# Optimization experiments

Measured on AMD Instinct MI355X. Metric: run time of the kernel, lower is better.

The kernel has to match this reference:

```python
import jax, jax.numpy as jnp
import numpy as np
from jax import lax
from jax.scipy.special import logsumexp

B, T, K, D = 16, 128, 1024, 768
APPROX_R = 0.1
LAMBD = 0.1
KP = int(APPROX_R * K)  # num_state_approx = 102


def setup_inputs() -> dict:
    key = jax.random.key(0)
    k0, k1, k2, k3 = jax.random.split(key, 4)
    x_emb = jax.random.normal(k0, (B, T, D), jnp.float32)
    # nn.Parameter(torch.normal(0, norm_scale_transition, [K, D]))
    state_matrix = 0.01 * jax.random.normal(k1, (K, D), jnp.float32)
    y = jax.random.randint(k2, (B, T), 0, K)
    y_lens = jax.random.randint(k3, (B,), 1, T + 1)
    return {"x_emb": x_emb, "state_matrix": state_matrix, "y": y, "y_lens": y_lens}


def _forward_sum(transition, emission, y_lens):
    # exact linear-chain CRF forward (logsumexp) scan. emission: [B,T,K]
    bsz = emission.shape[0]
    def step(alpha, em_t):
        new = logsumexp(alpha[:, :, None] + transition[None], axis=1) + em_t
        return new, new
    a0 = emission[:, 0]
    _, rest = lax.scan(step, a0, jnp.swapaxes(emission, 0, 1)[1:])
    alphas = jnp.concatenate([a0[None], rest], axis=0)  # [T,B,K]
    a_last = alphas[y_lens - 1, jnp.arange(bsz)]        # [B,K]
    return logsumexp(a_last, axis=-1)


def _approx_forward(state_matrix, emission, y_lens, kp):
    # restricted forward over the top-kp states (by emission potential) per
    # position; transitions among selected states computed on the fly from
    # state embeddings (avoids the full KxK transition).
    bsz = emission.shape[0]
    d = state_matrix.shape[1]
    em_top, idx = lax.top_k(emission, kp)   # [B,T,KP]
    st_sel = state_matrix[idx]              # [B,T,KP,D]
    def step(carry, inp):
        alpha, st_prev = carry
        em_t, st_t = inp
        trans_t = jnp.einsum('bid,bjd->bij', st_prev, st_t) / np.sqrt(d)
        new = logsumexp(alpha[:, :, None] + trans_t, axis=1) + em_t
        return (new, st_t), new
    a0 = em_top[:, 0]
    xs = (jnp.swapaxes(em_top, 0, 1)[1:], jnp.swapaxes(st_sel, 0, 1)[1:])
    _, rest = lax.scan(step, (a0, st_sel[:, 0]), xs)
    alphas = jnp.concatenate([a0[None], rest], axis=0)
    a_last = alphas[y_lens - 1, jnp.arange(bsz)]
    return logsumexp(a_last, axis=-1)


def _viterbi(transition, emission, y_lens):
    bsz, tlen, k = emission.shape
    def step(alpha, em_t):
        scores = alpha[:, :, None] + transition[None]
        bp = jnp.argmax(scores, axis=1).astype(jnp.int32)
        new = jnp.max(scores, axis=1) + em_t
        return new, (new, bp)
    a0 = emission[:, 0]
    _, (rest, bps) = lax.scan(step, a0, jnp.swapaxes(emission, 0, 1)[1:])
    alphas = jnp.concatenate([a0[None], rest], axis=0)  # [T,B,K]
    a_last = alphas[y_lens - 1, jnp.arange(bsz)]
    last_state = jnp.argmax(a_last, axis=-1).astype(jnp.int32)
    # bps[t] maps best state at t+1 -> state at t; pad to length T
    bps_pad = jnp.concatenate([bps, jnp.zeros((1, bsz, k), jnp.int32)], axis=0)
    def back(s, inp):
        t, bp_t = inp
        cand = jnp.take_along_axis(bp_t, s[:, None], axis=1)[:, 0]
        s_new = jnp.where(t == y_lens - 1, last_state,
                          jnp.where(t < y_lens - 1, cand, 0))
        return s_new, s_new
    ts = jnp.arange(tlen)[::-1]
    _, s_seq = lax.scan(back, jnp.zeros((bsz,), jnp.int32), (ts, bps_pad[::-1]))
    return jnp.swapaxes(s_seq[::-1], 0, 1)  # [B,T]


def _evaluate(y_pred, y, y_lens, mask_f):
    support = ((y > 0).astype(jnp.float32) * mask_f).sum()
    pred = ((y_pred > 0).astype(jnp.float32) * mask_f).sum()
    overlap = (((y_pred > 0) & (y > 0)).astype(jnp.float32) * mask_f).sum()
    acc = ((y_pred == y).astype(jnp.float32) * mask_f).sum() / y_lens.sum()
    prec = jnp.where(pred > 0, overlap / jnp.maximum(pred, 1.0), 0.0)
    recl = overlap / jnp.maximum(support, 1.0)
    f1 = jnp.where(prec > 0, 2 * prec * recl / jnp.maximum(prec + recl, 1e-12), 0.0)
    return acc, prec, recl, f1


def reference(x_emb, state_matrix, y, y_lens):
    d = x_emb.shape[-1]
    bsz, tlen = y.shape
    emission = jnp.einsum('btd,kd->btk', x_emb, state_matrix) / np.sqrt(d)
    transition = jnp.matmul(state_matrix, state_matrix.T) / np.sqrt(d)

    log_Z = _forward_sum(transition, emission, y_lens)
    log_Z_approx = _approx_forward(state_matrix, emission, y_lens, KP)

    # gold sequence log potential, masked by lengths
    pos = jnp.arange(tlen)
    mask = (pos[None, :] < y_lens[:, None])
    mask_f = mask.astype(jnp.float32)
    mask_tr = (pos[None, :tlen - 1] < (y_lens - 1)[:, None]).astype(jnp.float32)
    em_y = jnp.take_along_axis(emission, y[..., None], axis=-1)[..., 0]
    trans_y = transition[y[:, :-1], y[:, 1:]]
    log_y_potential = (em_y * mask_f).sum(-1) + (trans_y * mask_tr).sum(-1)

    seq_log_prob_exact = -(log_y_potential - log_Z).mean()
    seq_log_prob_approx = -(log_y_potential - log_Z_approx).mean()

    total_len = y_lens.sum()
    logp = jax.nn.log_softmax(emission, axis=-1)
    lp_y = jnp.take_along_axis(logp, y[..., None], axis=-1)[..., 0]
    seq_log_prob_local = (lp_y * mask_f).sum() / total_len
    max_prob = (jnp.max(jax.nn.softmax(emission, -1), -1) * mask_f).sum() / total_len

    # loss_type == 'approx_crf'
    loss = seq_log_prob_approx + LAMBD * seq_log_prob_local

    crf_output = _viterbi(transition, emission, y_lens)
    crf_acc, crf_prec, crf_recl, crf_f1 = _evaluate(crf_output, y, y_lens, mask_f)
    softmax_output = emission.argmax(-1)
    sm_acc, sm_prec, sm_recl, sm_f1 = _evaluate(softmax_output, y, y_lens, mask_f)

    return (loss, crf_output, log_Z.mean(), log_Z_approx.mean(),
            seq_log_prob_exact, seq_log_prob_local, max_prob,
            crf_acc, crf_f1, sm_acc, sm_f1)


if __name__ == '__main__':
    out = reference(**setup_inputs())
    print(out[0], out[2], out[3])
```

## Files before the change

kernel.cpp:

```cpp
#include <hip/hip_runtime.h>
#include <cstdint>
#include <cstddef>

typedef unsigned long long ull;
typedef unsigned int uint32;
typedef unsigned short u16;
typedef __attribute__((ext_vector_type(8))) short s8v;
typedef __attribute__((ext_vector_type(4))) float f32x4;


#define OFF_EM    ((size_t)0)
#define OFF_TR    ((size_t)2097152)
#define OFF_EXPTB ((size_t)3145728)
#define OFF_UPP   ((size_t)3670016)
#define OFF_APP   ((size_t)3735552)
#define OFF_ULST  ((size_t)3801088)
#define OFF_ALST  ((size_t)3817472)
#define OFF_UALST ((size_t)3833856)
#define OFF_ETOP  ((size_t)3835904)
#define OFF_ITOP  ((size_t)4044800)
#define OFF_RMAX  ((size_t)4253696)
#define OFF_RLSE  ((size_t)4255744)
#define OFF_SMP   ((size_t)4257792)
#define OFF_BP    ((size_t)4259840)
#define OFF_DONE  ((size_t)6356992)
#define OFF_EXPTT ((size_t)6367744)

__device__ __forceinline__ u16 f2bf(float f) {
  uint32 u = __builtin_bit_cast(uint32, f);
  u = (u + 0x7fffu + ((u >> 16) & 1u)) >> 16;
  return (u16)u;
}
__device__ __forceinline__ float bflo(uint32 w) {
  return __builtin_bit_cast(float, w << 16);
}
__device__ __forceinline__ void bfsplit(float v, u16& h, u16& l) {
  h = f2bf(v);
  float rh = __builtin_bit_cast(float, ((uint32)h) << 16);
  l = f2bf(v - rh);
}

__device__ __forceinline__ uint32 load_bypass_u32(const uint32* p) {
  return __hip_atomic_load(p, __ATOMIC_RELAXED, __HIP_MEMORY_SCOPE_AGENT);
}
__device__ __forceinline__ void store_bypass_u32(uint32* p, uint32 v) {
  __hip_atomic_store(p, v, __ATOMIC_RELAXED, __HIP_MEMORY_SCOPE_AGENT);
}
__device__ __forceinline__ void store_bypass_u16(u16* p, u16 v) {
  __hip_atomic_store(p, v, __ATOMIC_RELAXED, __HIP_MEMORY_SCOPE_AGENT);
}
__device__ __forceinline__ float load_bypass_f(const float* p) {
  return __hip_atomic_load(p, __ATOMIC_RELAXED, __HIP_MEMORY_SCOPE_AGENT);
}
__device__ __forceinline__ void store_bypass_f(float* p, float v) {
  __hip_atomic_store(p, v, __ATOMIC_RELAXED, __HIP_MEMORY_SCOPE_AGENT);
}
__device__ __forceinline__ void store_bypass_i(int* p, int v) {
  __hip_atomic_store(p, v, __ATOMIC_RELAXED, __HIP_MEMORY_SCOPE_AGENT);
}
__device__ __forceinline__ int load_bypass_i(const int* p) {
  return __hip_atomic_load(p, __ATOMIC_RELAXED, __HIP_MEMORY_SCOPE_AGENT);
}
__device__ __forceinline__ void cnt_add(uint32* p) {
  __hip_atomic_fetch_add(p, 1u, __ATOMIC_RELAXED, __HIP_MEMORY_SCOPE_AGENT);
}
__device__ __forceinline__ float4 ld_b128_sc1(const float4* p) {
  float4 r;
  asm volatile("global_load_dwordx4 %0, %1, off sc1" : "=v"(r) : "v"(p));
  return r;
}

__global__ __launch_bounds__(256) void gemm_kernel(
    const float* __restrict__ x, const float* __restrict__ stm,
    float* __restrict__ emission, float* __restrict__ transition,
    u16* __restrict__ expTb) {
  __shared__ float As[16][68];
  __shared__ float Bs[16][68];
  const int tid = threadIdx.x;
  const int tx = tid & 15, ty = tid >> 4;
  const int m0 = blockIdx.x * 64, n0 = blockIdx.y * 64;
  const int lr = tid >> 2;
  const int lc = (tid & 3) << 2;
  float acc[4][4] = {};
  const float* aptr;
  {
    int gr = m0 + lr;
    aptr = (gr < 2048) ? (x + (size_t)gr * 768) : (stm + (size_t)(gr - 2048) * 768);
  }
  const float* bptr = stm + (size_t)(n0 + lr) * 768;
  for (int k0 = 0; k0 < 768; k0 += 16) {
    float4 a4 = *(const float4*)(aptr + k0 + lc);
    float4 b4 = *(const float4*)(bptr + k0 + lc);
    __syncthreads();
    As[lc + 0][lr] = a4.x; As[lc + 1][lr] = a4.y; As[lc + 2][lr] = a4.z; As[lc + 3][lr] = a4.w;
    Bs[lc + 0][lr] = b4.x; Bs[lc + 1][lr] = b4.y; Bs[lc + 2][lr] = b4.z; Bs[lc + 3][lr] = b4.w;
    __syncthreads();
#pragma unroll
    for (int kk = 0; kk < 16; ++kk) {
      float a[4], b[4];
#pragma unroll
      for (int q = 0; q < 4; ++q) a[q] = As[kk][ty * 4 + q];
#pragma unroll
      for (int q = 0; q < 4; ++q) b[q] = Bs[kk][tx * 4 + q];
#pragma unroll
      for (int i2 = 0; i2 < 4; ++i2)
#pragma unroll
        for (int j2 = 0; j2 < 4; ++j2) acc[i2][j2] += a[i2] * b[j2];
    }
  }
  const float rs = 0.03608439182435161f;
#pragma unroll
  for (int i2 = 0; i2 < 4; ++i2) {
    int r = m0 + ty * 4 + i2;
#pragma unroll
    for (int j2 = 0; j2 < 4; ++j2) {
      int c = n0 + tx * 4 + j2;
      float v = acc[i2][j2] * rs;
      if (r < 2048) {
        emission[(size_t)r * 1024 + c] = v;
      } else {
        size_t o = (size_t)(r - 2048) * 1024 + c;
        transition[o] = v;
        expTb[o] = f2bf(expf(v));
      }
    }
  }
}

__global__ __launch_bounds__(256) void transT_kernel(
    const u16* __restrict__ src, u16* __restrict__ dst) {
  __shared__ u16 tile[64][65];
  const int bx = blockIdx.x * 64, by = blockIdx.y * 64;
  const int tx = threadIdx.x & 63, ty4 = threadIdx.x >> 6;
  for (int rr = ty4; rr < 64; rr += 4)
    tile[rr][tx] = src[(size_t)(bx + rr) * 1024 + by + tx];
  __syncthreads();
  for (int rr = ty4; rr < 64; rr += 4)
    dst[(size_t)(by + rr) * 1024 + bx + tx] = tile[tx][rr];
}

__global__ __launch_bounds__(256) void topk_kernel(
    const float* __restrict__ emission, float* __restrict__ em_top,
    int* __restrict__ top_idx, float* __restrict__ row_max,
    float* __restrict__ row_lse, int* __restrict__ sm_pred) {
  __shared__ float v[1024];
  __shared__ int ix[1024];
  __shared__ float rb[256];
  const int row = blockIdx.x;
  const int tid = threadIdx.x;
  const float* e = emission + (size_t)row * 1024;
  for (int p = tid; p < 1024; p += 256) { v[p] = e[p]; ix[p] = p; }
  __syncthreads();
  for (int k = 2; k <= 1024; k <<= 1) {
    for (int j = k >> 1; j > 0; j >>= 1) {
      for (int p = tid; p < 1024; p += 256) {
        int l = p ^ j;
        if (l > p) {
          float va = v[p], vb = v[l];
          int ia = ix[p], ib = ix[l];
          bool aBefore = (va > vb) || (va == vb && ia < ib);
          bool up = ((p & k) == 0);
          if (up ? !aBefore : aBefore) { v[p] = vb; v[l] = va; ix[p] = ib; ix[l] = ia; }
        }
      }
      __syncthreads();
    }
  }
  float mx = v[0];
  float s = 0.f;
  for (int p = tid; p < 1024; p += 256) s += expf(v[p] - mx);
  rb[tid] = s; __syncthreads();
  for (int w = 128; w > 0; w >>= 1) { if (tid < w) rb[tid] += rb[tid + w]; __syncthreads(); }
  if (tid == 0) {
    row_max[row] = mx;
    row_lse[row] = mx + logf(rb[0]);
    sm_pred[row] = ix[0];
  }
  for (int p = tid; p < 102; p += 256) {
    em_top[(size_t)row * 102 + p] = v[p];
    top_idx[(size_t)row * 102 + p] = ix[p];
  }
}

__global__ __launch_bounds__(256) void zero_kernel(uint32* __restrict__ done) {
  const int idx = blockIdx.x * 256 + threadIdx.x;
  store_bypass_u32(done + idx, 0u);
}

__global__ __launch_bounds__(512) void scan_kernel(
    const float* __restrict__ em, const float* __restrict__ tr,
    const u16* __restrict__ expTb, const u16* __restrict__ expTbT,
    const float* __restrict__ em_top, const int* __restrict__ top_idx,
    const int* __restrict__ y_lens,
    float* __restrict__ u_ring, float* __restrict__ av_ring,
    float* __restrict__ u_last, float* __restrict__ av_last,
    float* __restrict__ ua_last, int* __restrict__ bp,
    uint32* __restrict__ done, float* __restrict__ out_crf) {
  __shared__ ull SH[9232];
  const int bid = blockIdx.x, tid = threadIdx.x;
  uint32* cntF = done;
  uint32* cntV = done + 64;
  uint32* vdone = done + 640;

  if (bid < 8) {
    const int p = bid;
    int* stbF = (int*)(SH + 8192);
    if (tid < 16) stbF[tid] = y_lens[tid] - 1;
    const int l = tid & 63;
    const int lm = l & 15, lq = l >> 4;
    const int w2 = (tid >> 6) & 3;
    if (tid < 256) {
      const int m = tid >> 4;
      const int nn = p * 128 + ((tid & 15) << 3);
      const float* e0 = em + ((size_t)m << 17) + nn;
      u16* rh = (u16*)u_ring;
      const bool last0 = (y_lens[m] == 1);
#pragma unroll
      for (int q = 0; q < 8; ++q) {
        float v = expf(e0[q]);
        u16 h, lo2; bfsplit(v, h, lo2);
        store_bypass_u16(rh + m * 1024 + nn + q, h);
        store_bypass_u16(rh + 16384 + m * 1024 + nn + q, lo2);
        if (last0) u_last[(size_t)m * 1024 + nn + q] = v;
      }
      asm volatile("s_waitcnt vmcnt(0)" ::: "memory");
    }
    __syncthreads();
    if (tid == 0) cnt_add(cntF + 0);
    const char* Ab = (const char*)SH;
    const int offh = (lm << 11) + (lq << 4);
    const int axor = (lm & 7) << 4;
    const int nbase = p * 128 + w2 * 32;
    const u16* bq0 = expTbT + ((size_t)(nbase + lm) << 10) + (lq << 3);
    const u16* bq1 = bq0 + (16 << 10);
    for (int t = 1; t < 128; ++t) {
      if (tid == 0) {
        const uint32 tgt = (uint32)((((t - 1) >> 2) + 1) * 8);
        const uint32* cp = cntF + (((t - 1) & 3) << 4);
        while (load_bypass_u32(cp) < tgt) __builtin_amdgcn_s_sleep(1);
      }
      __syncthreads();
      {
        const float4* src = (const float4*)(u_ring + (size_t)((t - 1) & 3) * 16384);
        float4 dbuf[8];
#pragma unroll
        for (int q = 0; q < 8; ++q) dbuf[q] = ld_b128_sc1(src + (q << 9) + tid);
        asm volatile("s_waitcnt vmcnt(0)" ::: "memory");
        __builtin_amdgcn_sched_barrier(0);
#pragma unroll
        for (int q = 0; q < 8; ++q) {
          const int ob = ((q << 9) + tid) << 4;
          *(float4*)((char*)SH + (ob ^ (((ob >> 11) & 7) << 4))) = dbuf[q];
        }
      }
      __syncthreads();
      if (tid < 256) {
        f32x4 acc0a = {0.f, 0.f, 0.f, 0.f}, acc0b = {0.f, 0.f, 0.f, 0.f};
        f32x4 acc1a = {0.f, 0.f, 0.f, 0.f}, acc1b = {0.f, 0.f, 0.f, 0.f};
        for (int k0 = 0; k0 < 1024; k0 += 64) {
          const int o0 = (offh + (k0 << 1)) ^ axor;
          const int o1 = (offh + ((k0 + 32) << 1)) ^ axor;
          s8v ah0 = *(const s8v*)(Ab + o0);
          s8v al0 = *(const s8v*)(Ab + 32768 + o0);
          s8v ah1 = *(const s8v*)(Ab + o1);
          s8v al1 = *(const s8v*)(Ab + 32768 + o1);
          s8v b00 = *(const s8v*)(bq0 + k0);
          s8v b10 = *(const s8v*)(bq1 + k0);
          s8v b01 = *(const s8v*)(bq0 + k0 + 32);
          s8v b11 = *(const s8v*)(bq1 + k0 + 32);
          acc0a = __builtin_amdgcn_mfma_f32_16x16x32_bf16(ah0, b00, acc0a, 0, 0, 0);
          acc1a = __builtin_amdgcn_mfma_f32_16x16x32_bf16(ah0, b10, acc1a, 0, 0, 0);
          acc0b = __builtin_amdgcn_mfma_f32_16x16x32_bf16(ah1, b01, acc0b, 0, 0, 0);
          acc1b = __builtin_amdgcn_mfma_f32_16x16x32_bf16(ah1, b11, acc1b, 0, 0, 0);
          acc0a = __builtin_amdgcn_mfma_f32_16x16x32_bf16(al0, b00, acc0a, 0, 0, 0);
          acc1a = __builtin_amdgcn_mfma_f32_16x16x32_bf16(al0, b10, acc1a, 0, 0, 0);
          acc0b = __builtin_amdgcn_mfma_f32_16x16x32_bf16(al1, b01, acc0b, 0, 0, 0);
          acc1b = __builtin_amdgcn_mfma_f32_16x16x32_bf16(al1, b11, acc1b, 0, 0, 0);
        }
        u16* rh = (u16*)(u_ring + (size_t)(t & 3) * 16384);
        const float sc = 1.0f / 1024.0f;
#pragma unroll
        for (int r = 0; r < 4; ++r) {
          const int m = (lq << 2) + r;
          const size_t erow = (((size_t)m << 7) + t) << 10;
          {
            const int n = nbase + lm;
            float v = (acc0a[r] + acc0b[r]) * sc * expf(em[erow + n]);
            u16 h, lo2; bfsplit(v, h, lo2);
            store_bypass_u16(rh + m * 1024 + n, h);
            store_bypass_u16(rh + 16384 + m * 1024 + n, lo2);
            if (t == stbF[m]) u_last[(size_t)m * 1024 + n] = v;
          }
          {
            const int n = nbase + 16 + lm;
            float v = (acc1a[r] + acc1b[r]) * sc * expf(em[erow + n]);
            u16 h, lo2; bfsplit(v, h, lo2);
            store_bypass_u16(rh + m * 1024 + n, h);
            store_bypass_u16(rh + 16384 + m * 1024 + n, lo2);
            if (t == stbF[m]) u_last[(size_t)m * 1024 + n] = v;
          }
        }
        asm volatile("s_waitcnt vmcnt(0)" ::: "memory");
      }
      __syncthreads();
      if (tid == 0) cnt_add(cntF + ((t & 3) << 4));
    }
  } else if (bid < 136) {
    const int v = bid - 8;
    const int n0v = ((v & 7) << 7) + ((v >> 3) << 3);
    const int jj = tid & 7, g = tid >> 3;
    const int col = n0v + jj;
    ull* ppb = (ull*)((char*)SH + 65536);
    int* stb2 = (int*)((char*)SH + 73728);
    if (tid < 16) stb2[tid] = y_lens[tid] - 1;
    if (tid < 128) {
      const int jb = tid & 7, b = tid >> 3;
      const float e0 = em[((size_t)b << 17) + n0v + jb];
      store_bypass_f(av_ring + (size_t)(n0v + jb) * 16 + b, e0);
      if (y_lens[b] == 1) store_bypass_f(av_last + ((size_t)b << 10) + n0v + jb, e0);
      asm volatile("s_waitcnt vmcnt(0)" ::: "memory");
    }
    __syncthreads();
    if (tid == 0) cnt_add(cntV + ((v & 7) << 4));
    const char* stc = (const char*)SH;
    for (int t = 1; t < 128; ++t) {
      if (tid < 8) {
        const uint32 tgt = (uint32)((((t - 1) >> 2) + 1) * 16);
        const uint32* cp = cntV + (((((t - 1) & 3) << 3) + tid) << 4);
        while (load_bypass_u32(cp) < tgt) __builtin_amdgcn_s_sleep(1);
      }
      __syncthreads();
      {
        const float4* src = (const float4*)(av_ring + (size_t)((t - 1) & 3) * 16384);
        float4 dbuf[8];
#pragma unroll
        for (int q = 0; q < 8; ++q) dbuf[q] = ld_b128_sc1(src + (q << 9) + tid);
        asm volatile("s_waitcnt vmcnt(0)" ::: "memory");
        __builtin_amdgcn_sched_barrier(0);
#pragma unroll
        for (int q = 0; q < 8; ++q) {
          const int ob = ((q << 9) + tid) << 4;
          *(float4*)((char*)SH + (ob ^ (((ob >> 10) & 7) << 4))) = dbuf[q];
        }
      }
      __syncthreads();
      float mv[16]; int mi[16];
#pragma unroll
      for (int b = 0; b < 16; ++b) { mv[b] = -3.0e38f; mi[b] = 0x7fffffff; }
      const float* trc = tr + col;
      const int i0 = g << 4;
#pragma unroll 4
      for (int ii = 0; ii < 16; ++ii) {
        const int i = i0 + ii;
        const float tv = trc[(size_t)i << 10];
        const int ph = (i << 6) ^ (((i >> 4) & 7) << 4);
        const f32x4 s0 = *(const f32x4*)(stc + (ph ^ 0));
        const f32x4 s1 = *(const f32x4*)(stc + (ph ^ 16));
        const f32x4 s2 = *(const f32x4*)(stc + (ph ^ 32));
        const f32x4 s3 = *(const f32x4*)(stc + (ph ^ 48));
#pragma unroll
        for (int b = 0; b < 4; ++b) {
          float c0 = s0[b] + tv; if (c0 > mv[b])      { mv[b] = c0;      mi[b] = i; }
          float c1 = s1[b] + tv; if (c1 > mv[b + 4])  { mv[b + 4] = c1;  mi[b + 4] = i; }
          float c2 = s2[b] + tv; if (c2 > mv[b + 8])  { mv[b + 8] = c2;  mi[b + 8] = i; }
          float c3 = s3[b] + tv; if (c3 > mv[b + 12]) { mv[b + 12] = c3; mi[b + 12] = i; }
        }
      }
#pragma unroll
      for (int d = 8; d <= 32; d <<= 1) {
#pragma unroll
        for (int b = 0; b < 16; ++b) {
          float ov = __shfl_xor(mv[b], d);
          int oi = __shfl_xor(mi[b], d);
          if (ov > mv[b] || (ov == mv[b] && oi < mi[b])) { mv[b] = ov; mi[b] = oi; }
        }
      }
      if ((tid & 63) < 8) {
        const int wv = tid >> 6;
#pragma unroll
        for (int b = 0; b < 16; ++b) {
          ull pk = ((ull)(uint32)mi[b] << 32) | (ull)__builtin_bit_cast(uint32, mv[b]);
          ppb[(b << 6) + (wv << 3) + jj] = pk;
        }
      }
      __syncthreads();
      if (tid < 128) {
        const int jb = tid & 7, b = tid >> 3;
        const int cf = n0v + jb;
        float bmv = -3.0e38f; int bmi = 0x7fffffff;
#pragma unroll
        for (int w = 0; w < 8; ++w) {
          ull pk = ppb[(b << 6) + (w << 3) + jb];
          float pv = __builtin_bit_cast(float, (uint32)pk);
          int pi = (int)(pk >> 32);
          if (pv > bmv || (pv == bmv && pi < bmi)) { bmv = pv; bmi = pi; }
        }
        const float nv = bmv + em[((((size_t)b << 7) + t) << 10) + cf];
        store_bypass_f(av_ring + (size_t)(t & 3) * 16384 + (size_t)cf * 16 + b, nv);
        store_bypass_i(bp + ((size_t)t << 14) + ((size_t)b << 10) + cf, bmi);
        if (t == stb2[b]) store_bypass_f(av_last + ((size_t)b << 10) + cf, nv);
        asm volatile("s_waitcnt vmcnt(0)" ::: "memory");
      }
      __syncthreads();
      if (tid == 0) cnt_add(cntV + ((((t & 3) << 3) + (v & 7)) << 4));
    }
    if (tid == 0) cnt_add(vdone);
    if (v == 0) {
      if (tid == 0) {
        while (load_bypass_u32(vdone) < 128u) __builtin_amdgcn_s_sleep(1);
      }
      __syncthreads();
      const int wv = tid >> 6, lh = tid & 63;
      const int hb = lh >> 5, hl = lh & 31;
      const int b = wv * 2 + hb;
      const int tbb = y_lens[b] - 1;
      for (int t2 = tbb + 1 + hl; t2 < 128; t2 += 32) out_crf[(b << 7) + t2] = 0.f;
      float bv = -3.0e38f; int bi = 0x7fffffff;
      for (int q = 0; q < 32; ++q) {
        const int i = (q << 5) + hl;
        const float val = load_bypass_f(av_last + ((size_t)b << 10) + i);
        if (val > bv || (val == bv && i < bi)) { bv = val; bi = i; }
      }
#pragma unroll
      for (int d = 1; d < 32; d <<= 1) {
        float ov = __shfl_xor(bv, d, 32);
        int oi = __shfl_xor(bi, d, 32);
        if (ov > bv || (ov == bv && oi < bi)) { bv = ov; bi = oi; }
      }
      if (hl == 0) {
        int sx = bi;
        out_crf[(b << 7) + tbb] = (float)sx;
        for (int t2 = tbb - 1; t2 >= 0; --t2) {
          sx = load_bypass_i(bp + ((size_t)(t2 + 1) << 14) + ((size_t)b << 10) + sx);
          out_crf[(b << 7) + t2] = (float)sx;
        }
      }
    }
  } else {
    const int b = bid - 136;
    const int tb = y_lens[b] - 1;
    const int j2 = tid & 127, h2 = tid >> 7;
    float* sua0 = (float*)SH;
    float* sua1 = sua0 + 104;
    int* sidxp = (int*)(sua0 + 208);
    int* sidxc = sidxp + 104;
    float* aps = (float*)(sidxc + 104);
    if (tid < 102) {
      float vv = expf(em_top[(size_t)(b * 128) * 102 + tid]);
      sua0[tid] = vv;
      if (tb == 0) ua_last[b * 102 + tid] = vv;
    }
    __syncthreads();
    for (int t = 1; t < 128; ++t) {
      if (tid < 102) sidxp[tid] = top_idx[((size_t)b * 128 + (t - 1)) * 102 + tid];
      else if (tid >= 256 && tid < 358)
        sidxc[tid - 256] = top_idx[((size_t)b * 128 + t) * 102 + (tid - 256)];
      __syncthreads();
      float acc2 = 0.f;
      float* up = (t & 1) ? sua0 : sua1;
      float* cur = (t & 1) ? sua1 : sua0;
      if (j2 < 102) {
        const int colc = sidxc[j2];
        const int ia = h2 * 26;
        const int ib2 = (ia + 26 < 102) ? ia + 26 : 102;
        for (int i = ia; i < ib2; ++i)
          acc2 += up[i] * bflo((uint32)expTb[(size_t)sidxp[i] * 1024 + colc]);
      }
      if (h2 > 0 && j2 < 102) aps[(h2 - 1) * 104 + j2] = acc2;
      __syncthreads();
      if (h2 == 0 && j2 < 102) {
        acc2 += aps[j2] + aps[104 + j2] + aps[208 + j2];
        const float e = em_top[((size_t)b * 128 + t) * 102 + j2];
        const float nv = acc2 * expf(e) * (1.0f / 102.0f);
        cur[j2] = nv;
        if (t == tb) ua_last[b * 102 + j2] = nv;
      }
      __syncthreads();
    }
  }
}

__device__ __forceinline__ float blk_sum(float v, float* rb, int tid) {
  rb[tid] = v; __syncthreads();
  for (int w = 128; w > 0; w >>= 1) { if (tid < w) rb[tid] += rb[tid + w]; __syncthreads(); }
  float r = rb[0]; __syncthreads();
  return r;
}

__global__ __launch_bounds__(256) void finalize_kernel(
    const float* __restrict__ emission, const float* __restrict__ transition,
    const float* __restrict__ u_last, const float* __restrict__ ua_last,
    const float* __restrict__ row_max, const float* __restrict__ row_lse,
    const int* __restrict__ sm_pred, const int* __restrict__ y,
    const int* __restrict__ y_lens, float* __restrict__ d_out) {
  __shared__ float rb[256];
  __shared__ float sZ[16], sZa[16], sLogy[16];
  const int tid = threadIdx.x;
  const float* out_crf = d_out + 1;
  for (int b = 0; b < 16; ++b) {
    const int tb = y_lens[b] - 1;
    float p = 0.f;
    for (int i = tid; i < 1024; i += 256) p += u_last[(size_t)b * 1024 + i];
    p = blk_sum(p, rb, tid);
    if (tid == 0) sZ[b] = logf(p) + (float)tb * 6.931471805599453f;
    float q = 0.f;
    for (int i = tid; i < 102; i += 256) q += ua_last[(size_t)b * 102 + i];
    q = blk_sum(q, rb, tid);
    if (tid == 0) sZa[b] = logf(q) + (float)tb * 4.624972813284271f;
  }
  if (tid < 16) sLogy[tid] = 0.f;
  __syncthreads();
  float a_local = 0, a_maxp = 0, c_sup = 0, c_pred = 0, c_ov = 0, c_match = 0;
  float s_predc = 0, s_ov = 0, s_match = 0;
  for (int r = tid; r < 2048; r += 256) {
    const int b = r >> 7, t = r & 127;
    const int L = y_lens[b];
    if (t < L) {
      const int yv = y[r];
      const float em_y = emission[(size_t)r * 1024 + yv];
      const float lse = row_lse[r];
      a_local += em_y - lse;
      a_maxp += expf(row_max[r] - lse);
      float term = em_y;
      if (t < L - 1) term += transition[(size_t)yv * 1024 + y[r + 1]];
      atomicAdd(&sLogy[b], term);
      const float ypos = (yv > 0) ? 1.f : 0.f;
      c_sup += ypos;
      const int cs = (int)out_crf[r];
      c_pred += (cs > 0) ? 1.f : 0.f;
      c_ov += ((cs > 0) && (yv > 0)) ? 1.f : 0.f;
      c_match += (cs == yv) ? 1.f : 0.f;
      const int ss = sm_pred[r];
      s_predc += (ss > 0) ? 1.f : 0.f;
      s_ov += ((ss > 0) && (yv > 0)) ? 1.f : 0.f;
      s_match += (ss == yv) ? 1.f : 0.f;
    }
  }
  __syncthreads();
  a_local = blk_sum(a_local, rb, tid);
  a_maxp = blk_sum(a_maxp, rb, tid);
  c_sup = blk_sum(c_sup, rb, tid);
  c_pred = blk_sum(c_pred, rb, tid);
  c_ov = blk_sum(c_ov, rb, tid);
  c_match = blk_sum(c_match, rb, tid);
  s_predc = blk_sum(s_predc, rb, tid);
  s_ov = blk_sum(s_ov, rb, tid);
  s_match = blk_sum(s_match, rb, tid);
  if (tid == 0) {
    float tl = 0.f;
    for (int b = 0; b < 16; ++b) tl += (float)y_lens[b];
    float mZ = 0, mZa = 0, dE = 0, dA = 0;
    for (int b = 0; b < 16; ++b) {
      mZ += sZ[b]; mZa += sZa[b];
      dE += sLogy[b] - sZ[b];
      dA += sLogy[b] - sZa[b];
    }
    mZ *= (1.f / 16.f); mZa *= (1.f / 16.f);
    const float sle = -dE * (1.f / 16.f);
    const float sla = -dA * (1.f / 16.f);
    const float slocal = a_local / tl;
    const float maxp = a_maxp / tl;
    const float loss = sla + 0.1f * slocal;
    const float crf_acc = c_match / tl;
    const float crf_prec = (c_pred > 0.f) ? (c_ov / fmaxf(c_pred, 1.f)) : 0.f;
    const float crf_recl = c_ov / fmaxf(c_sup, 1.f);
    const float crf_f1 = (crf_prec > 0.f)
        ? (2.f * crf_prec * crf_recl / fmaxf(crf_prec + crf_recl, 1e-12f)) : 0.f;
    const float sm_acc = s_match / tl;
    const float sm_prec = (s_predc > 0.f) ? (s_ov / fmaxf(s_predc, 1.f)) : 0.f;
    const float sm_recl = s_ov / fmaxf(c_sup, 1.f);
    const float sm_f1 = (sm_prec > 0.f)
        ? (2.f * sm_prec * sm_recl / fmaxf(sm_prec + sm_recl, 1e-12f)) : 0.f;
    d_out[0] = loss;
    d_out[2049] = mZ;
    d_out[2050] = mZa;
    d_out[2051] = sle;
    d_out[2052] = slocal;
    d_out[2053] = maxp;
    d_out[2054] = crf_acc;
    d_out[2055] = crf_f1;
    d_out[2056] = sm_acc;
    d_out[2057] = sm_f1;
  }
}

extern "C" void kernel_launch(void* const* d_in, const int* in_sizes, int n_in,
                              void* d_out, int out_size, void* d_ws, size_t ws_size,
                              hipStream_t stream) {
  const float* x = (const float*)d_in[0];
  const float* stm = (const float*)d_in[1];
  const int* y = (const int*)d_in[2];
  const int* yl = (const int*)d_in[3];
  float* out = (float*)d_out;
  float* ws = (float*)d_ws;

  float* emission = ws + OFF_EM;
  float* transition = ws + OFF_TR;
  u16* expTb = (u16*)(ws + OFF_EXPTB);
  u16* expTbT = (u16*)(ws + OFF_EXPTT);
  float* u_ring = ws + OFF_UPP;
  float* av_ring = ws + OFF_APP;
  float* u_last = ws + OFF_ULST;
  float* av_last = ws + OFF_ALST;
  float* ua_last = ws + OFF_UALST;
  float* em_top = ws + OFF_ETOP;
  int* top_idx = (int*)(ws + OFF_ITOP);
  float* row_max = ws + OFF_RMAX;
  float* row_lse = ws + OFF_RLSE;
  int* sm_pred = (int*)(ws + OFF_SMP);
  int* bp = (int*)(ws + OFF_BP);
  uint32* done = (uint32*)(ws + OFF_DONE);

  zero_kernel<<<4, 256, 0, stream>>>(done);
  gemm_kernel<<<dim3(48, 16), 256, 0, stream>>>(x, stm, emission, transition, expTb);
  transT_kernel<<<dim3(16, 16), 256, 0, stream>>>(expTb, expTbT);
  topk_kernel<<<2048, 256, 0, stream>>>(emission, em_top, top_idx, row_max, row_lse, sm_pred);
  scan_kernel<<<152, 512, 0, stream>>>(emission, transition, expTb, expTbT, em_top, top_idx,
                                       yl, u_ring, av_ring, u_last, av_last, ua_last,
                                       bp, done, out + 1);
  finalize_kernel<<<1, 256, 0, stream>>>(emission, transition, u_last, ua_last,
                                         row_max, row_lse, sm_pred, y, yl, out);
}
```

Before: 1.887 ms.

## Replace counter-based inter-block sync with poisoned ring-buffer data flags

Drops the per-step atomic counters and spin-waits in the persistent scan kernel. Consumers now reload ring-buffer entries until none holds a poison sentinel, and each block re-poisons the slot two steps ahead. The forward ring also packs the bf16 hi/lo halves into one 32-bit word, halving the number of stores, and the consumer unpacks them into LDS. This removes the store drain, barrier and atomic round-trip on every step, but relies on relaxed store visibility ordering and on the sentinel never colliding with real data.

```diff
diff --git a/kernel.cpp b/kernel.cpp
--- a/kernel.cpp
+++ b/kernel.cpp
@@ -8,6 +8,9 @@
 typedef __attribute__((ext_vector_type(8))) short s8v;
 typedef __attribute__((ext_vector_type(4))) float f32x4;
 
+
+#define POISON32 0xFFFFFFFFu
+#define POISON64 0xFFFFFFFFFFFFFFFFull
 
 #define OFF_EM    ((size_t)0)
 #define OFF_TR    ((size_t)2097152)
@@ -46,7 +49,7 @@
 __device__ __forceinline__ void store_bypass_u32(uint32* p, uint32 v) {
   __hip_atomic_store(p, v, __ATOMIC_RELAXED, __HIP_MEMORY_SCOPE_AGENT);
 }
-__device__ __forceinline__ void store_bypass_u16(u16* p, u16 v) {
+__device__ __forceinline__ void store_bypass_u64(ull* p, ull v) {
   __hip_atomic_store(p, v, __ATOMIC_RELAXED, __HIP_MEMORY_SCOPE_AGENT);
 }
 __device__ __forceinline__ float load_bypass_f(const float* p) {
@@ -182,9 +185,12 @@
   }
 }
 
-__global__ __launch_bounds__(256) void zero_kernel(uint32* __restrict__ done) {
+__global__ __launch_bounds__(256) void poison_kernel(
+    ull* __restrict__ uring, ull* __restrict__ aring, uint32* __restrict__ done) {
   const int idx = blockIdx.x * 256 + threadIdx.x;
-  store_bypass_u32(done + idx, 0u);
+  store_bypass_u64(uring + idx, POISON64);
+  store_bypass_u64(aring + idx, POISON64);
+  if (idx == 0) store_bypass_u32(done, 0u);
 }
 
 __global__ __launch_bounds__(512) void scan_kernel(
@@ -198,9 +204,7 @@
     uint32* __restrict__ done, float* __restrict__ out_crf) {
   __shared__ ull SH[9232];
   const int bid = blockIdx.x, tid = threadIdx.x;
-  uint32* cntF = done;
-  uint32* cntV = done + 64;
-  uint32* vdone = done + 640;
+  uint32* vdone = done;
 
   if (bid < 8) {
     const int p = bid;
@@ -213,20 +217,17 @@
       const int m = tid >> 4;
       const int nn = p * 128 + ((tid & 15) << 3);
       const float* e0 = em + ((size_t)m << 17) + nn;
-      u16* rh = (u16*)u_ring;
+      uint32* rw = (uint32*)u_ring;
       const bool last0 = (y_lens[m] == 1);
 #pragma unroll
       for (int q = 0; q < 8; ++q) {
         float v = expf(e0[q]);
         u16 h, lo2; bfsplit(v, h, lo2);
-        store_bypass_u16(rh + m * 1024 + nn + q, h);
-        store_bypass_u16(rh + 16384 + m * 1024 + nn + q, lo2);
+        store_bypass_u32(rw + m * 1024 + nn + q, ((uint32)lo2 << 16) | h);
         if (last0) u_last[(size_t)m * 1024 + nn + q] = v;
       }
-      asm volatile("s_waitcnt vmcnt(0)" ::: "memory");
     }
     __syncthreads();
-    if (tid == 0) cnt_add(cntF + 0);
     const char* Ab = (const char*)SH;
     const int offh = (lm << 11) + (lq << 4);
     const int axor = (lm & 7) << 4;
@@ -234,26 +235,49 @@
     const u16* bq0 = expTbT + ((size_t)(nbase + lm) << 10) + (lq << 3);
     const u16* bq1 = bq0 + (16 << 10);
     for (int t = 1; t < 128; ++t) {
-      if (tid == 0) {
-        const uint32 tgt = (uint32)((((t - 1) >> 2) + 1) * 8);
-        const uint32* cp = cntF + (((t - 1) & 3) << 4);
-        while (load_bypass_u32(cp) < tgt) __builtin_amdgcn_s_sleep(1);
-      }
-      __syncthreads();
       {
         const float4* src = (const float4*)(u_ring + (size_t)((t - 1) & 3) * 16384);
         float4 dbuf[8];
 #pragma unroll
         for (int q = 0; q < 8; ++q) dbuf[q] = ld_b128_sc1(src + (q << 9) + tid);
         asm volatile("s_waitcnt vmcnt(0)" ::: "memory");
+#pragma unroll
+        for (int q = 0; q < 8; ++q) {
+          uint4 w = __builtin_bit_cast(uint4, dbuf[q]);
+          while (w.x == POISON32 || w.y == POISON32 ||
+                 w.z == POISON32 || w.w == POISON32) {
+            __builtin_amdgcn_s_sleep(1);
+            dbuf[q] = ld_b128_sc1(src + (q << 9) + tid);
+            asm volatile("s_waitcnt vmcnt(0)" ::: "memory");
+            w = __builtin_bit_cast(uint4, dbuf[q]);
+          }
+          dbuf[q] = __builtin_bit_cast(float4, w);
+        }
         __builtin_amdgcn_sched_barrier(0);
 #pragma unroll
         for (int q = 0; q < 8; ++q) {
-          const int ob = ((q << 9) + tid) << 4;
-          *(float4*)((char*)SH + (ob ^ (((ob >> 11) & 7) << 4))) = dbuf[q];
-        }
-      }
-      __syncthreads();
+          const uint4 w = __builtin_bit_cast(uint4, dbuf[q]);
+          const uint32 h01 = (w.x & 0xffffu) | (w.y << 16);
+          const uint32 h23 = (w.z & 0xffffu) | (w.w << 16);
+          const uint32 l01 = (w.x >> 16) | (w.y & 0xffff0000u);
+          const uint32 l23 = (w.z >> 16) | (w.w & 0xffff0000u);
+          const int hb = ((q << 9) + tid) << 3;
+          *(ull*)((char*)SH + (hb ^ (((hb >> 11) & 7) << 4))) = ((ull)h23 << 32) | h01;
+          const int lb = 32768 + hb;
+          *(ull*)((char*)SH + (lb ^ (((lb >> 11) & 7) << 4))) = ((ull)l23 << 32) | l01;
+        }
+      }
+      __syncthreads();
+      if (tid >= 256) {
+        uint32* pz = (uint32*)u_ring + (size_t)((t + 2) & 3) * 16384;
+        const int ti = tid - 256;
+#pragma unroll
+        for (int q = 0; q < 8; ++q) {
+          const int r = ti * 8 + q;
+          store_bypass_u32(pz + ((r >> 7) << 10) + p * 128 + (r & 127), POISON32);
+        }
+        asm volatile("s_waitcnt vmcnt(0)" ::: "memory");
+      }
       if (tid < 256) {
         f32x4 acc0a = {0.f, 0.f, 0.f, 0.f}, acc0b = {0.f, 0.f, 0.f, 0.f};
         f32x4 acc1a = {0.f, 0.f, 0.f, 0.f}, acc1b = {0.f, 0.f, 0.f, 0.f};
@@ -277,7 +301,7 @@
           acc0b = __builtin_amdgcn_mfma_f32_16x16x32_bf16(al1, b01, acc0b, 0, 0, 0);
           acc1b = __builtin_amdgcn_mfma_f32_16x16x32_bf16(al1, b11, acc1b, 0, 0, 0);
         }
-        u16* rh = (u16*)(u_ring + (size_t)(t & 3) * 16384);
+        uint32* rw = (uint32*)u_ring + (size_t)(t & 3) * 16384;
         const float sc = 1.0f / 1024.0f;
 #pragma unroll
         for (int r = 0; r < 4; ++r) {
@@ -287,23 +311,19 @@
             const int n = nbase + lm;
             float v = (acc0a[r] + acc0b[r]) * sc * expf(em[erow + n]);
             u16 h, lo2; bfsplit(v, h, lo2);
-            store_bypass_u16(rh + m * 1024 + n, h);
-            store_bypass_u16(rh + 16384 + m * 1024 + n, lo2);
+            store_bypass_u32(rw + m * 1024 + n, ((uint32)lo2 << 16) | h);
             if (t == stbF[m]) u_last[(size_t)m * 1024 + n] = v;
           }
           {
             const int n = nbase + 16 + lm;
             float v = (acc1a[r] + acc1b[r]) * sc * expf(em[erow + n]);
             u16 h, lo2; bfsplit(v, h, lo2);
-            store_bypass_u16(rh + m * 1024 + n, h);
-            store_bypass_u16(rh + 16384 + m * 1024 + n, lo2);
+            store_bypass_u32(rw + m * 1024 + n, ((uint32)lo2 << 16) | h);
             if (t == stbF[m]) u_last[(size_t)m * 1024 + n] = v;
           }
         }
-        asm volatile("s_waitcnt vmcnt(0)" ::: "memory");
-      }
-      __syncthreads();
-      if (tid == 0) cnt_add(cntF + ((t & 3) << 4));
+      }
+      __syncthreads();
     }
   } else if (bid < 136) {
     const int v = bid - 8;
@@ -318,24 +338,28 @@
       const float e0 = em[((size_t)b << 17) + n0v + jb];
       store_bypass_f(av_ring + (size_t)(n0v + jb) * 16 + b, e0);
       if (y_lens[b] == 1) store_bypass_f(av_last + ((size_t)b << 10) + n0v + jb, e0);
-      asm volatile("s_waitcnt vmcnt(0)" ::: "memory");
     }
     __syncthreads();
-    if (tid == 0) cnt_add(cntV + ((v & 7) << 4));
     const char* stc = (const char*)SH;
     for (int t = 1; t < 128; ++t) {
-      if (tid < 8) {
-        const uint32 tgt = (uint32)((((t - 1) >> 2) + 1) * 16);
-        const uint32* cp = cntV + (((((t - 1) & 3) << 3) + tid) << 4);
-        while (load_bypass_u32(cp) < tgt) __builtin_amdgcn_s_sleep(1);
-      }
-      __syncthreads();
       {
         const float4* src = (const float4*)(av_ring + (size_t)((t - 1) & 3) * 16384);
         float4 dbuf[8];
 #pragma unroll
         for (int q = 0; q < 8; ++q) dbuf[q] = ld_b128_sc1(src + (q << 9) + tid);
         asm volatile("s_waitcnt vmcnt(0)" ::: "memory");
+#pragma unroll
+        for (int q = 0; q < 8; ++q) {
+          uint4 w = __builtin_bit_cast(uint4, dbuf[q]);
+          while (w.x == POISON32 || w.y == POISON32 ||
+                 w.z == POISON32 || w.w == POISON32) {
+            __builtin_amdgcn_s_sleep(1);
+            dbuf[q] = ld_b128_sc1(src + (q << 9) + tid);
+            asm volatile("s_waitcnt vmcnt(0)" ::: "memory");
+            w = __builtin_bit_cast(uint4, dbuf[q]);
+          }
+          dbuf[q] = __builtin_bit_cast(float4, w);
+        }
         __builtin_amdgcn_sched_barrier(0);
 #pragma unroll
         for (int q = 0; q < 8; ++q) {
@@ -344,6 +368,12 @@
         }
       }
       __syncthreads();
+      if (tid < 32) {
+        uint32* pz = (uint32*)av_ring + (size_t)((t + 2) & 3) * 16384 + n0v * 16;
+#pragma unroll
+        for (int q = 0; q < 4; ++q) store_bypass_u32(pz + tid * 4 + q, POISON32);
+        asm volatile("s_waitcnt vmcnt(0)" ::: "memory");
+      }
       float mv[16]; int mi[16];
 #pragma unroll
       for (int b = 0; b < 16; ++b) { mv[b] = -3.0e38f; mi[b] = 0x7fffffff; }
@@ -399,11 +429,11 @@
         store_bypass_f(av_ring + (size_t)(t & 3) * 16384 + (size_t)cf * 16 + b, nv);
         store_bypass_i(bp + ((size_t)t << 14) + ((size_t)b << 10) + cf, bmi);
         if (t == stb2[b]) store_bypass_f(av_last + ((size_t)b << 10) + cf, nv);
-        asm volatile("s_waitcnt vmcnt(0)" ::: "memory");
-      }
-      __syncthreads();
-      if (tid == 0) cnt_add(cntV + ((((t & 3) << 3) + (v & 7)) << 4));
-    }
+      }
+      __syncthreads();
+    }
+    asm volatile("s_waitcnt vmcnt(0)" ::: "memory");
+    __syncthreads();
     if (tid == 0) cnt_add(vdone);
     if (v == 0) {
       if (tid == 0) {
@@ -611,7 +641,7 @@
   int* bp = (int*)(ws + OFF_BP);
   uint32* done = (uint32*)(ws + OFF_DONE);
 
-  zero_kernel<<<4, 256, 0, stream>>>(done);
+  poison_kernel<<<128, 256, 0, stream>>>((ull*)u_ring, (ull*)av_ring, done);
   gemm_kernel<<<dim3(48, 16), 256, 0, stream>>>(x, stm, emission, transition, expTb);
   transT_kernel<<<dim3(16, 16), 256, 0, stream>>>(expTb, expTbT);
   topk_kernel<<<2048, 256, 0, stream>>>(emission, em_top, top_idx, row_max, row_lse, sm_pred);
```

After: 1.908 ms. About the same (+1.1%).
